# Optimization experiments

Hardware: AMD Instinct MI355X
Metric: run time of the kernel (lower is better)

## Reference

```python
import jax, jax.numpy as jnp
import numpy as np

N_NODES = 20000
EPS_BN = 1e-5
NEG_SLOPE = 0.2


def gat_conv(x, W, att_src, att_dst, bias, src, dst, heads, out_ch, concat):
    n = x.shape[0]
    h = (x @ W).reshape(n, heads, out_ch)                       # [N,H,C]
    a_src = jnp.sum(h * att_src, axis=-1)                       # [N,H]
    a_dst = jnp.sum(h * att_dst, axis=-1)                       # [N,H]
    e = jax.nn.leaky_relu(a_src[src] + a_dst[dst], NEG_SLOPE)   # [E,H]
    # segment softmax over incoming edges of each destination node
    m = jax.ops.segment_max(e, dst, num_segments=n)             # [N,H]
    e = jnp.exp(e - m[dst])
    denom = jax.ops.segment_sum(e, dst, num_segments=n)         # [N,H]
    alpha = e / (denom[dst] + 1e-16)                            # [E,H]
    msg = alpha[:, :, None] * h[src]                            # [E,H,C]
    out = jax.ops.segment_sum(msg, dst, num_segments=n)         # [N,H,C]
    if concat:
        out = out.reshape(n, heads * out_ch)
    else:
        out = out.mean(axis=1)
    return out + bias


def batch_norm(x, gamma, beta):
    mu = x.mean(axis=0)
    var = x.var(axis=0)  # biased, matches torch normalization
    return (x - mu) * jax.lax.rsqrt(var + EPS_BN) * gamma + beta


def setup_inputs() -> dict:
    key = jax.random.key(0)
    ks = jax.random.split(key, 16)
    n, d_in, hid, heads = N_NODES, 768, 128, 8
    n_edges = 160000
    x = jax.random.normal(ks[0], (n, d_in), dtype=jnp.float32)
    edge_index = jax.random.randint(ks[1], (2, n_edges), 0, n, dtype=jnp.int64)
    s = lambda fi, fo: (2.0 / (fi + fo)) ** 0.5
    return {
        "x": x,
        "edge_index": edge_index,
        "W1": jax.random.normal(ks[2], (d_in, heads * hid), jnp.float32) * s(d_in, heads * hid),
        "att_src1": jax.random.normal(ks[3], (heads, hid), jnp.float32) * 0.1,
        "att_dst1": jax.random.normal(ks[4], (heads, hid), jnp.float32) * 0.1,
        "bias1": jnp.zeros((heads * hid,), jnp.float32),
        "bn1_g": jnp.ones((heads * hid,), jnp.float32),
        "bn1_b": jnp.zeros((heads * hid,), jnp.float32),
        "W2": jax.random.normal(ks[5], (heads * hid, hid), jnp.float32) * s(heads * hid, hid),
        "att_src2": jax.random.normal(ks[6], (1, hid), jnp.float32) * 0.1,
        "att_dst2": jax.random.normal(ks[7], (1, hid), jnp.float32) * 0.1,
        "bias2": jnp.zeros((hid,), jnp.float32),
        "bn2_g": jnp.ones((hid,), jnp.float32),
        "bn2_b": jnp.zeros((hid,), jnp.float32),
        "Wc1": jax.random.normal(ks[8], (hid, 64), jnp.float32) * s(hid, 64),
        "bc1": jnp.zeros((64,), jnp.float32),
        "Wc2": jax.random.normal(ks[9], (64, 2), jnp.float32) * s(64, 2),
        "bc2": jnp.zeros((2,), jnp.float32),
    }


def reference(x, edge_index, W1, att_src1, att_dst1, bias1, bn1_g, bn1_b,
              W2, att_src2, att_dst2, bias2, bn2_g, bn2_b,
              Wc1, bc1, Wc2, bc2):
    n = x.shape[0]
    # PyG GATConv default: add self-loops
    loops = jnp.arange(n, dtype=edge_index.dtype)
    src = jnp.concatenate([edge_index[0], loops])
    dst = jnp.concatenate([edge_index[1], loops])

    h = gat_conv(x, W1, att_src1, att_dst1, bias1, src, dst, heads=8, out_ch=128, concat=True)
    h = jax.nn.elu(batch_norm(h, bn1_g, bn1_b))
    # dropout disabled (deterministic reference)
    h = gat_conv(h, W2, att_src2, att_dst2, bias2, src, dst, heads=1, out_ch=128, concat=False)
    h = jax.nn.elu(batch_norm(h, bn2_g, bn2_b))
    h = jax.nn.elu(h @ Wc1 + bc1)
    return h @ Wc2 + bc2  # [N, 2] logits
```

## Files before the change

### kernel.cpp

```cpp
#include <hip/hip_runtime.h>
#include <stdint.h>

typedef unsigned short u16;
typedef __bf16 bf16x8 __attribute__((ext_vector_type(8)));
typedef float f32x4 __attribute__((ext_vector_type(4)));

__device__ __forceinline__ float b2f(u16 u) {
    unsigned x = ((unsigned)u) << 16;
    return __builtin_bit_cast(float, x);
}
__device__ __forceinline__ u16 f2b(float f) {
    unsigned x = __builtin_bit_cast(unsigned, f);
    x = x + 0x7fffu + ((x >> 16) & 1u);
    return (u16)(x >> 16);
}
__device__ __forceinline__ float leaky(float v) { return v > 0.f ? v : 0.2f * v; }

__device__ __forceinline__ void gload16(const u16* g, u16* l) {
    __builtin_amdgcn_global_load_lds((const __attribute__((address_space(1))) void*)(const void*)g,
                                     (__attribute__((address_space(3))) void*)(void*)l, 16, 0, 0);
}

__global__ void k_cast4(const float* __restrict__ in, u16* __restrict__ out, size_t n4) {
    size_t i = blockIdx.x * (size_t)blockDim.x + threadIdx.x;
    size_t stride = (size_t)gridDim.x * blockDim.x;
    for (; i < n4; i += stride) {
        float4 v = ((const float4*)in)[i];
        ushort4 o;
        o.x = f2b(v.x); o.y = f2b(v.y); o.z = f2b(v.z); o.w = f2b(v.w);
        ((ushort4*)out)[i] = o;
    }
}

__global__ void k_tcast(const float* __restrict__ in, u16* __restrict__ out, int R, int C) {
    __shared__ float tile[32][33];
    int tx = threadIdx.x & 31, ty = threadIdx.x >> 5;
    int c0 = blockIdx.x * 32, r0 = blockIdx.y * 32;
    #pragma unroll
    for (int i = 0; i < 32; i += 8) {
        int r = r0 + ty + i, c = c0 + tx;
        tile[ty + i][tx] = (r < R && c < C) ? in[(size_t)r * C + c] : 0.f;
    }
    __syncthreads();
    #pragma unroll
    for (int i = 0; i < 32; i += 8) {
        int c = c0 + ty + i, r = r0 + tx;
        if (c < C && r < R) out[(size_t)c * R + r] = f2b(tile[tx][ty + i]);
    }
}

#define GBM 128
#define GBN 128
#define GBK 64

__global__ __launch_bounds__(256) void k_gemm(const u16* __restrict__ A, const u16* __restrict__ Bt,
                                              u16* __restrict__ C, int M, int NN, int K,
                                              const float* __restrict__ attS, const float* __restrict__ attD,
                                              float* __restrict__ asrc, float* __restrict__ adst, int HEADS) {
    __shared__ __align__(16) u16 As[GBM][GBK];
    __shared__ __align__(16) u16 Bs[GBN][GBK];
    __shared__ float redS[4][64];
    __shared__ float redD[4][64];
    int brow = blockIdx.x * GBM, bcol = blockIdx.y * GBN;
    int t = threadIdx.x, lane = t & 63, wid = t >> 6;
    int wm = (wid >> 1) * 64, wn = (wid & 1) * 64;
    int fr = lane & 15, fq = lane >> 4;
    f32x4 acc[4][4] = {};
    int srow = lane >> 3;
    int scol = (lane & 7) * 8;
    int nK = K / GBK;
    for (int kt = 0; kt < nK; ++kt) {
        int k0 = kt * GBK;
        #pragma unroll
        for (int cc = 0; cc < 8; ++cc) {
            int c = wid * 8 + cc;
            int r = (c & 15) * 8 + srow;
            if (c < 16) gload16(A + (size_t)(brow + r) * K + k0 + scol, &As[r][scol]);
            else        gload16(Bt + (size_t)(bcol + r) * K + k0 + scol, &Bs[r][scol]);
        }
        __syncthreads();
        #pragma unroll
        for (int kk = 0; kk < 2; ++kk) {
            int ko = kk * 32 + fq * 8;
            bf16x8 af[4], bg[4];
            #pragma unroll
            for (int i = 0; i < 4; ++i) {
                af[i] = *reinterpret_cast<const bf16x8*>(&As[wm + i * 16 + fr][ko]);
                bg[i] = *reinterpret_cast<const bf16x8*>(&Bs[wn + i * 16 + fr][ko]);
            }
            #pragma unroll
            for (int mi = 0; mi < 4; ++mi)
                #pragma unroll
                for (int ni = 0; ni < 4; ++ni)
                    acc[mi][ni] = __builtin_amdgcn_mfma_f32_16x16x32_bf16(af[mi], bg[ni], acc[mi][ni], 0, 0, 0);
        }
        __syncthreads();
    }
    #pragma unroll
    for (int mi = 0; mi < 4; ++mi) {
        #pragma unroll
        for (int j = 0; j < 4; ++j) {
            int row = brow + wm + mi * 16 + fq * 4 + j;
            if (row < M) {
                #pragma unroll
                for (int ni = 0; ni < 4; ++ni) {
                    int col = bcol + wn + ni * 16 + fr;
                    C[(size_t)row * NN + col] = f2b(acc[mi][ni][j]);
                }
            }
        }
    }
    if (attS != nullptr) {
        int head = blockIdx.y;
        const float* sv = attS + head * 128;
        const float* dv = attD + head * 128;
        float ps[4][4], pd[4][4];
        #pragma unroll
        for (int mi = 0; mi < 4; ++mi)
            #pragma unroll
            for (int j = 0; j < 4; ++j) {
                float s = 0.f, d = 0.f;
                #pragma unroll
                for (int ni = 0; ni < 4; ++ni) {
                    int lc = wn + ni * 16 + fr;
                    s += acc[mi][ni][j] * sv[lc];
                    d += acc[mi][ni][j] * dv[lc];
                }
                ps[mi][j] = s; pd[mi][j] = d;
            }
        #pragma unroll
        for (int mask = 1; mask < 16; mask <<= 1)
            #pragma unroll
            for (int mi = 0; mi < 4; ++mi)
                #pragma unroll
                for (int j = 0; j < 4; ++j) {
                    ps[mi][j] += __shfl_xor(ps[mi][j], mask);
                    pd[mi][j] += __shfl_xor(pd[mi][j], mask);
                }
        if (fr == 0) {
            #pragma unroll
            for (int mi = 0; mi < 4; ++mi)
                #pragma unroll
                for (int j = 0; j < 4; ++j) {
                    redS[wid][mi * 16 + fq * 4 + j] = ps[mi][j];
                    redD[wid][mi * 16 + fq * 4 + j] = pd[mi][j];
                }
        }
        __syncthreads();
        if ((wid & 1) == 0) {
            int row = brow + wm + lane;
            if (row < M) {
                asrc[(size_t)row * HEADS + head] = redS[wid][lane] + redS[wid | 1][lane];
                adst[(size_t)row * HEADS + head] = redD[wid][lane] + redD[wid | 1][lane];
            }
        }
    }
}

__global__ void k_detect(const int* __restrict__ ei, int* flag, int E0) {
    if (threadIdx.x == 0) *flag = 0;
    __syncthreads();
    int lim = E0 < 4096 ? E0 : 4096;
    int any = 0;
    for (int i = threadIdx.x; i < lim; i += 256) any |= (ei[2 * i + 1] != 0);
    if (any) atomicOr(flag, 1);
}

__global__ void k_deg(const int* __restrict__ ei, const int* __restrict__ flag,
                      int* __restrict__ deg, int E0, int E) {
    bool i64 = (*flag == 0);
    for (int e = blockIdx.x * blockDim.x + threadIdx.x; e < E; e += gridDim.x * blockDim.x) {
        int d;
        if (e < E0) d = i64 ? ei[2 * (E0 + e)] : ei[E0 + e];
        else d = e - E0;
        atomicAdd(&deg[d], 1);
    }
}

__global__ __launch_bounds__(1024) void k_scan(const int* __restrict__ deg, int* __restrict__ off,
                                               int* __restrict__ cursor, int n) {
    __shared__ int part[1024];
    int t = threadIdx.x;
    int chunk = (n + 1023) >> 10;
    int beg = t * chunk, end = beg + chunk;
    if (end > n) end = n;
    int s = 0;
    for (int i = beg; i < end; ++i) s += deg[i];
    part[t] = s;
    __syncthreads();
    for (int d = 1; d < 1024; d <<= 1) {
        int v = (t >= d) ? part[t - d] : 0;
        __syncthreads();
        part[t] += v;
        __syncthreads();
    }
    int run = (t == 0) ? 0 : part[t - 1];
    for (int i = beg; i < end; ++i) { off[i] = run; cursor[i] = run; run += deg[i]; }
    if (t == 1023) off[n] = part[1023];
}

__global__ void k_scatter(const int* __restrict__ ei, const int* __restrict__ flag,
                          int* __restrict__ cursor, int* __restrict__ csr, int E0, int E) {
    bool i64 = (*flag == 0);
    for (int e = blockIdx.x * blockDim.x + threadIdx.x; e < E; e += gridDim.x * blockDim.x) {
        int s, d;
        if (e < E0) {
            if (i64) { s = ei[2 * e]; d = ei[2 * (E0 + e)]; }
            else     { s = ei[e];     d = ei[E0 + e]; }
        } else { s = d = e - E0; }
        int pos = atomicAdd(&cursor[d], 1);
        csr[pos] = s;
    }
}

template <int HEADS>
__global__ __launch_bounds__(256) void k_alpha(const int* __restrict__ off, const int* __restrict__ csr,
                                               const float* __restrict__ asrc, const float* __restrict__ adst,
                                               float* __restrict__ pbuf, float* __restrict__ invb, int N) {
    const int EPC = 64 / HEADS;
    int t = threadIdx.x, lane = t & 63, wid = t >> 6;
    int node = blockIdx.x * 4 + wid;
    if (node >= N) return;
    int h = lane & (HEADS - 1);
    int e = lane / HEADS;
    float ad = adst[(size_t)node * HEADS + h];
    int lo = off[node], hi = off[node + 1];
    float m = -1e30f;
    for (int i = lo + e; i < hi; i += EPC) {
        int s = csr[i];
        float v = leaky(asrc[(size_t)s * HEADS + h] + ad);
        m = fmaxf(m, v);
    }
    #pragma unroll
    for (int mask = HEADS; mask < 64; mask <<= 1) m = fmaxf(m, __shfl_xor(m, mask));
    float ssum = 0.f;
    for (int i = lo + e; i < hi; i += EPC) {
        int s = csr[i];
        float v = leaky(asrc[(size_t)s * HEADS + h] + ad);
        float p = __expf(v - m);
        pbuf[(size_t)i * HEADS + h] = p;
        ssum += p;
    }
    #pragma unroll
    for (int mask = HEADS; mask < 64; mask <<= 1) ssum += __shfl_xor(ssum, mask);
    if (lane < HEADS) invb[(size_t)node * HEADS + h] = 1.f / (ssum + 1e-16f);
}

__global__ __launch_bounds__(256) void k_agg1(const int* __restrict__ off, const int* __restrict__ csr,
                                              const float* __restrict__ pbuf, const float* __restrict__ invb,
                                              const u16* __restrict__ h1, u16* __restrict__ outg, int N) {
    int node = blockIdx.x;
    if (node >= N) return;
    int t = threadIdx.x;
    int hh = t >> 5;
    int c0 = t * 4;
    int lo = off[node], hi = off[node + 1];
    float a0 = 0.f, a1 = 0.f, a2 = 0.f, a3 = 0.f;
    for (int i = lo; i < hi; ++i) {
        int s = csr[i];
        float p = pbuf[(size_t)i * 8 + hh];
        ushort4 u = *(const ushort4*)(h1 + (size_t)s * 1024 + c0);
        a0 += p * b2f(u.x); a1 += p * b2f(u.y);
        a2 += p * b2f(u.z); a3 += p * b2f(u.w);
    }
    float inv = invb[(size_t)node * 8 + hh];
    ushort4 o;
    o.x = f2b(a0 * inv); o.y = f2b(a1 * inv); o.z = f2b(a2 * inv); o.w = f2b(a3 * inv);
    *(ushort4*)(outg + (size_t)node * 1024 + c0) = o;
}

__global__ __launch_bounds__(256) void k_agg2(const int* __restrict__ off, const int* __restrict__ csr,
                                              const float* __restrict__ pbuf, const float* __restrict__ invb,
                                              const u16* __restrict__ h2, u16* __restrict__ outg, int N) {
    int t = threadIdx.x;
    int half = t >> 7, c = t & 127;
    int node = blockIdx.x * 2 + half;
    if (node >= N) return;
    int lo = off[node], hi = off[node + 1];
    float acc = 0.f;
    for (int i = lo; i < hi; ++i) {
        int s = csr[i];
        acc += pbuf[i] * b2f(h2[(size_t)s * 128 + c]);
    }
    outg[(size_t)node * 128 + c] = f2b(acc * invb[node]);
}

template <int CH>
__global__ __launch_bounds__(256) void k_bnpart(const u16* __restrict__ g, float* __restrict__ ps,
                                                float* __restrict__ ps2, int Nrows, int rowsPerChunk) {
    const int TPR = CH / 4;
    const int RPI = 256 / TPR;
    int t = threadIdx.x;
    int rl = t / TPR, c4 = (t % TPR) * 4;
    int chunk = blockIdx.x;
    int r0 = chunk * rowsPerChunk;
    int r1 = r0 + rowsPerChunk; if (r1 > Nrows) r1 = Nrows;
    float s[4] = {0.f, 0.f, 0.f, 0.f}, s2[4] = {0.f, 0.f, 0.f, 0.f};
    for (int r = r0 + rl; r < r1; r += RPI) {
        ushort4 u = *(const ushort4*)(g + (size_t)r * CH + c4);
        float v0 = b2f(u.x), v1 = b2f(u.y), v2 = b2f(u.z), v3 = b2f(u.w);
        s[0] += v0; s2[0] += v0 * v0;
        s[1] += v1; s2[1] += v1 * v1;
        s[2] += v2; s2[2] += v2 * v2;
        s[3] += v3; s2[3] += v3 * v3;
    }
    size_t prow = (size_t)(chunk * RPI + rl) * CH + c4;
    *(float4*)(ps + prow)  = make_float4(s[0], s[1], s[2], s[3]);
    *(float4*)(ps2 + prow) = make_float4(s2[0], s2[1], s2[2], s2[3]);
}

__global__ __launch_bounds__(256) void k_bnfinal(const float* __restrict__ ps, const float* __restrict__ ps2,
                                                 const float* __restrict__ gamma, const float* __restrict__ beta,
                                                 float* __restrict__ scale, float* __restrict__ shift,
                                                 int P, int CH, int Nrows) {
    int t = threadIdx.x, lane = t & 63, wid = t >> 6;
    int col = blockIdx.x * 4 + wid;
    if (col >= CH) return;
    float s = 0.f, s2 = 0.f;
    for (int p = lane; p < P; p += 64) {
        s += ps[(size_t)p * CH + col];
        s2 += ps2[(size_t)p * CH + col];
    }
    #pragma unroll
    for (int m = 1; m < 64; m <<= 1) { s += __shfl_xor(s, m); s2 += __shfl_xor(s2, m); }
    if (lane == 0) {
        double mu = (double)s / Nrows;
        double var = (double)s2 / Nrows - mu * mu;
        if (var < 0) var = 0;
        float sc = gamma[col] * rsqrtf((float)var + 1e-5f);
        scale[col] = sc;
        shift[col] = beta[col] - (float)mu * sc;
    }
}

__global__ void k_bn_elu(u16* __restrict__ g, const float* __restrict__ scale,
                         const float* __restrict__ shift, size_t total4, int CH) {
    size_t i = blockIdx.x * (size_t)blockDim.x + threadIdx.x;
    size_t stride = (size_t)gridDim.x * blockDim.x;
    for (; i < total4; i += stride) {
        size_t i4 = i * 4;
        int c0 = (int)(i4 % CH);
        ushort4 u = *(ushort4*)(g + i4);
        float v[4] = {b2f(u.x), b2f(u.y), b2f(u.z), b2f(u.w)};
        #pragma unroll
        for (int j = 0; j < 4; ++j) {
            float y = v[j] * scale[c0 + j] + shift[c0 + j];
            v[j] = y > 0.f ? y : expm1f(y);
        }
        ushort4 o;
        o.x = f2b(v[0]); o.y = f2b(v[1]); o.z = f2b(v[2]); o.w = f2b(v[3]);
        *(ushort4*)(g + i4) = o;
    }
}

__global__ __launch_bounds__(256) void k_cls(const u16* __restrict__ g2raw,
                                             const float* __restrict__ scale2, const float* __restrict__ shift2,
                                             const float* __restrict__ Wc1, const float* __restrict__ bc1,
                                             const float* __restrict__ Wc2, const float* __restrict__ bc2,
                                             float* __restrict__ out, int N) {
    __shared__ float wl[128 * 64];
    __shared__ float hs[4][128];
    int t = threadIdx.x, lane = t & 63, wid = t >> 6;
    for (int i = t; i < 128 * 64; i += 256) wl[i] = Wc1[i];
    float sc0 = scale2[2 * lane], sc1 = scale2[2 * lane + 1];
    float sh0 = shift2[2 * lane], sh1 = shift2[2 * lane + 1];
    float bb = bc1[lane];
    float c2a = Wc2[lane * 2], c2b = Wc2[lane * 2 + 1];
    float o2a = bc2[0], o2b = bc2[1];
    __syncthreads();
    int row0 = blockIdx.x * 64;
    for (int it = 0; it < 16; ++it) {
        int row = row0 + it * 4 + wid;
        if (row >= N) continue;
        const u16* hp = g2raw + (size_t)row * 128 + 2 * lane;
        float y0 = b2f(hp[0]) * sc0 + sh0; y0 = y0 > 0.f ? y0 : expm1f(y0);
        float y1 = b2f(hp[1]) * sc1 + sh1; y1 = y1 > 0.f ? y1 : expm1f(y1);
        hs[wid][2 * lane] = y0;
        hs[wid][2 * lane + 1] = y1;
        float tj = bb;
        #pragma unroll 8
        for (int c = 0; c < 128; ++c) tj += hs[wid][c] * wl[c * 64 + lane];
        tj = tj > 0.f ? tj : expm1f(tj);
        float v0 = tj * c2a, v1 = tj * c2b;
        #pragma unroll
        for (int m = 1; m < 64; m <<= 1) { v0 += __shfl_xor(v0, m); v1 += __shfl_xor(v1, m); }
        if (lane == 0) {
            out[(size_t)row * 2 + 0] = v0 + o2a;
            out[(size_t)row * 2 + 1] = v1 + o2b;
        }
    }
}

extern "C" void kernel_launch(void* const* d_in, const int* in_sizes, int n_in,
                              void* d_out, int out_size, void* d_ws, size_t ws_size,
                              hipStream_t stream) {
    const float* x     = (const float*)d_in[0];
    const int*   ei    = (const int*)d_in[1];
    const float* W1    = (const float*)d_in[2];
    const float* attS1 = (const float*)d_in[3];
    const float* attD1 = (const float*)d_in[4];
    const float* bn1g  = (const float*)d_in[6];
    const float* bn1b  = (const float*)d_in[7];
    const float* W2    = (const float*)d_in[8];
    const float* attS2 = (const float*)d_in[9];
    const float* attD2 = (const float*)d_in[10];
    const float* bn2g  = (const float*)d_in[12];
    const float* bn2b  = (const float*)d_in[13];
    const float* Wc1   = (const float*)d_in[14];
    const float* bc1   = (const float*)d_in[15];
    const float* Wc2   = (const float*)d_in[16];
    const float* bc2   = (const float*)d_in[17];
    float* out = (float*)d_out;

    const int DIN = 768, F1 = 1024, C2 = 128;
    const int N = in_sizes[0] / DIN;
    const int Mp = (N + GBM - 1) / GBM * GBM;
    const int E0 = in_sizes[1] / 2;
    const int E = E0 + N;

    char* w = (char*)d_ws;
    auto take = [&](size_t bytes) -> void* {
        void* p = (void*)w;
        w += (bytes + 255) & ~(size_t)255;
        return p;
    };
    u16* bufA   = (u16*)take((size_t)Mp * F1 * 2);
    u16* h1b    = (u16*)take((size_t)N * F1 * 2);
    u16* w1t    = (u16*)take((size_t)F1 * DIN * 2);
    u16* w2t    = (u16*)take((size_t)C2 * F1 * 2);
    float* asrc1 = (float*)take((size_t)N * 8 * 4);
    float* adst1 = (float*)take((size_t)N * 8 * 4);
    int* deg    = (int*)take((size_t)N * 4);
    int* off    = (int*)take((size_t)(N + 1) * 4);
    int* cursor = (int*)take((size_t)N * 4);
    int* csr    = (int*)take((size_t)E * 4);
    int* flag   = (int*)take(256);
    u16* h2b    = (u16*)take((size_t)N * C2 * 2);
    float* asrc2 = (float*)take((size_t)N * 4);
    float* adst2 = (float*)take((size_t)N * 4);
    u16* g2     = (u16*)take((size_t)N * C2 * 2);
    float* scale1 = (float*)take(F1 * 4);
    float* shift1 = (float*)take(F1 * 4);
    float* scale2 = (float*)take(C2 * 4);
    float* shift2 = (float*)take(C2 * 4);
    float* pbuf  = (float*)take((size_t)E * 8 * 4);
    float* invb1 = (float*)take((size_t)N * 8 * 4);
    float* invb2 = (float*)take((size_t)N * 4);
    float* psA   = (float*)take((size_t)1024 * 1024 * 4);
    float* psB   = (float*)take((size_t)1024 * 1024 * 4);

    hipMemsetAsync(deg, 0, (size_t)N * 4, stream);
    k_detect<<<1, 256, 0, stream>>>(ei, flag, E0);

    k_cast4<<<2048, 256, 0, stream>>>(x, bufA, (size_t)N * DIN / 4);
    k_tcast<<<dim3(F1 / 32, DIN / 32), 256, 0, stream>>>(W1, w1t, DIN, F1);
    k_tcast<<<dim3(C2 / 32, F1 / 32), 256, 0, stream>>>(W2, w2t, F1, C2);
    k_gemm<<<dim3(Mp / GBM, F1 / GBN), 256, 0, stream>>>(bufA, w1t, h1b, N, F1, DIN,
                                                         attS1, attD1, asrc1, adst1, 8);

    k_deg<<<512, 256, 0, stream>>>(ei, flag, deg, E0, E);
    k_scan<<<1, 1024, 0, stream>>>(deg, off, cursor, N);
    k_scatter<<<512, 256, 0, stream>>>(ei, flag, cursor, csr, E0, E);

    k_alpha<8><<<(N + 3) / 4, 256, 0, stream>>>(off, csr, asrc1, adst1, pbuf, invb1, N);
    k_agg1<<<N, 256, 0, stream>>>(off, csr, pbuf, invb1, h1b, bufA, N);
    {
        int nchunk = 256, rpc = (N + nchunk - 1) / nchunk;
        k_bnpart<1024><<<nchunk, 256, 0, stream>>>(bufA, psA, psB, N, rpc);
        k_bnfinal<<<F1 / 4, 256, 0, stream>>>(psA, psB, bn1g, bn1b, scale1, shift1, nchunk, F1, N);
    }
    k_bn_elu<<<4096, 256, 0, stream>>>(bufA, scale1, shift1, (size_t)N * F1 / 4, F1);

    k_gemm<<<dim3(Mp / GBM, C2 / GBN), 256, 0, stream>>>(bufA, w2t, h2b, N, C2, F1,
                                                         attS2, attD2, asrc2, adst2, 1);
    k_alpha<1><<<(N + 3) / 4, 256, 0, stream>>>(off, csr, asrc2, adst2, pbuf, invb2, N);
    k_agg2<<<(N + 1) / 2, 256, 0, stream>>>(off, csr, pbuf, invb2, h2b, g2, N);
    {
        int nchunk = 128, rpc = (N + nchunk - 1) / nchunk;
        k_bnpart<128><<<nchunk, 256, 0, stream>>>(g2, psA, psB, N, rpc);
        k_bnfinal<<<C2 / 4, 256, 0, stream>>>(psA, psB, bn2g, bn2b, scale2, shift2, nchunk * 8, C2, N);
    }

    k_cls<<<(N + 63) / 64, 256, 0, stream>>>(g2, scale2, shift2, Wc1, bc1, Wc2, bc2, out, N);
}
```

Before: 417.4 us.

## Fuse input cast and BN+ELU into GEMM A-loads; split attention dots out

The first GEMM now reads fp32 x directly and converts to bf16 while staging into LDS, which removes the separate cast kernel. The second GEMM applies the batch-norm scale/shift and ELU while loading A, which removes the standalone bn_elu pass over the 20000x1024 activation. Tile loads switch from async global_load_lds to register-staged loads into padded LDS rows, and the attention-score epilogue moves into separate small kernels that re-read h. The trade-offs are extra per-element ALU work in the GEMM load path, repeated transforms of A across column blocks, and the loss of direct-to-LDS loads.

```diff
diff --git a/kernel.cpp b/kernel.cpp
--- a/kernel.cpp
+++ b/kernel.cpp
@@ -15,22 +15,7 @@
     return (u16)(x >> 16);
 }
 __device__ __forceinline__ float leaky(float v) { return v > 0.f ? v : 0.2f * v; }
-
-__device__ __forceinline__ void gload16(const u16* g, u16* l) {
-    __builtin_amdgcn_global_load_lds((const __attribute__((address_space(1))) void*)(const void*)g,
-                                     (__attribute__((address_space(3))) void*)(void*)l, 16, 0, 0);
-}
-
-__global__ void k_cast4(const float* __restrict__ in, u16* __restrict__ out, size_t n4) {
-    size_t i = blockIdx.x * (size_t)blockDim.x + threadIdx.x;
-    size_t stride = (size_t)gridDim.x * blockDim.x;
-    for (; i < n4; i += stride) {
-        float4 v = ((const float4*)in)[i];
-        ushort4 o;
-        o.x = f2b(v.x); o.y = f2b(v.y); o.z = f2b(v.z); o.w = f2b(v.w);
-        ((ushort4*)out)[i] = o;
-    }
-}
+__device__ __forceinline__ float elu(float v) { return v > 0.f ? v : expm1f(v); }
 
 __global__ void k_tcast(const float* __restrict__ in, u16* __restrict__ out, int R, int C) {
     __shared__ float tile[32][33];
@@ -52,31 +37,68 @@
 #define GBM 128
 #define GBN 128
 #define GBK 64
-
-__global__ __launch_bounds__(256) void k_gemm(const u16* __restrict__ A, const u16* __restrict__ Bt,
+#define LDT 72
+
+template <int AMODE>
+__global__ __launch_bounds__(256) void k_gemm(const void* __restrict__ Araw, const u16* __restrict__ Bt,
                                               u16* __restrict__ C, int M, int NN, int K,
-                                              const float* __restrict__ attS, const float* __restrict__ attD,
-                                              float* __restrict__ asrc, float* __restrict__ adst, int HEADS) {
-    __shared__ __align__(16) u16 As[GBM][GBK];
-    __shared__ __align__(16) u16 Bs[GBN][GBK];
-    __shared__ float redS[4][64];
-    __shared__ float redD[4][64];
+                                              const float* __restrict__ scA, const float* __restrict__ shA) {
+    __shared__ __align__(16) u16 As[GBM][LDT];
+    __shared__ __align__(16) u16 Bs[GBN][LDT];
     int brow = blockIdx.x * GBM, bcol = blockIdx.y * GBN;
-    int t = threadIdx.x, lane = t & 63, wid = t >> 6;
+    int t = threadIdx.x;
+    int lane = t & 63, wid = t >> 6;
     int wm = (wid >> 1) * 64, wn = (wid & 1) * 64;
     int fr = lane & 15, fq = lane >> 4;
     f32x4 acc[4][4] = {};
-    int srow = lane >> 3;
-    int scol = (lane & 7) * 8;
+    int tr = t >> 3, tc = (t & 7) * 8;
     int nK = K / GBK;
     for (int kt = 0; kt < nK; ++kt) {
         int k0 = kt * GBK;
         #pragma unroll
-        for (int cc = 0; cc < 8; ++cc) {
-            int c = wid * 8 + cc;
-            int r = (c & 15) * 8 + srow;
-            if (c < 16) gload16(A + (size_t)(brow + r) * K + k0 + scol, &As[r][scol]);
-            else        gload16(Bt + (size_t)(bcol + r) * K + k0 + scol, &Bs[r][scol]);
+        for (int rr = 0; rr < 4; ++rr) {
+            int r = tr + rr * 32;
+            int grow = brow + r;
+            uint4 bv = *reinterpret_cast<const uint4*>(Bt + (size_t)(bcol + r) * K + k0 + tc);
+            *reinterpret_cast<uint4*>(&Bs[r][tc]) = bv;
+            uint4 av = make_uint4(0, 0, 0, 0);
+            if (AMODE == 0) {
+                if (grow < M) av = *reinterpret_cast<const uint4*>((const u16*)Araw + (size_t)grow * K + k0 + tc);
+            } else if (AMODE == 1) {
+                if (grow < M) {
+                    const float* ap = (const float*)Araw + (size_t)grow * K + k0 + tc;
+                    float4 a0 = *(const float4*)ap;
+                    float4 a1 = *(const float4*)(ap + 4);
+                    ushort4 lo, hi;
+                    lo.x = f2b(a0.x); lo.y = f2b(a0.y); lo.z = f2b(a0.z); lo.w = f2b(a0.w);
+                    hi.x = f2b(a1.x); hi.y = f2b(a1.y); hi.z = f2b(a1.z); hi.w = f2b(a1.w);
+                    av.x = (unsigned)lo.x | ((unsigned)lo.y << 16);
+                    av.y = (unsigned)lo.z | ((unsigned)lo.w << 16);
+                    av.z = (unsigned)hi.x | ((unsigned)hi.y << 16);
+                    av.w = (unsigned)hi.z | ((unsigned)hi.w << 16);
+                }
+            } else {
+                if (grow < M) {
+                    uint4 u = *reinterpret_cast<const uint4*>((const u16*)Araw + (size_t)grow * K + k0 + tc);
+                    float4 s0 = *(const float4*)(scA + k0 + tc);
+                    float4 s1 = *(const float4*)(scA + k0 + tc + 4);
+                    float4 h0 = *(const float4*)(shA + k0 + tc);
+                    float4 h1 = *(const float4*)(shA + k0 + tc + 4);
+                    u16 w0 = f2b(elu(b2f((u16)(u.x & 0xffff)) * s0.x + h0.x));
+                    u16 w1 = f2b(elu(b2f((u16)(u.x >> 16))    * s0.y + h0.y));
+                    u16 w2 = f2b(elu(b2f((u16)(u.y & 0xffff)) * s0.z + h0.z));
+                    u16 w3 = f2b(elu(b2f((u16)(u.y >> 16))    * s0.w + h0.w));
+                    u16 w4 = f2b(elu(b2f((u16)(u.z & 0xffff)) * s1.x + h1.x));
+                    u16 w5 = f2b(elu(b2f((u16)(u.z >> 16))    * s1.y + h1.y));
+                    u16 w6 = f2b(elu(b2f((u16)(u.w & 0xffff)) * s1.z + h1.z));
+                    u16 w7 = f2b(elu(b2f((u16)(u.w >> 16))    * s1.w + h1.w));
+                    av.x = (unsigned)w0 | ((unsigned)w1 << 16);
+                    av.y = (unsigned)w2 | ((unsigned)w3 << 16);
+                    av.z = (unsigned)w4 | ((unsigned)w5 << 16);
+                    av.w = (unsigned)w6 | ((unsigned)w7 << 16);
+                }
+            }
+            *reinterpret_cast<uint4*>(&As[r][tc]) = av;
         }
         __syncthreads();
         #pragma unroll
@@ -110,51 +132,45 @@
             }
         }
     }
-    if (attS != nullptr) {
-        int head = blockIdx.y;
-        const float* sv = attS + head * 128;
-        const float* dv = attD + head * 128;
-        float ps[4][4], pd[4][4];
-        #pragma unroll
-        for (int mi = 0; mi < 4; ++mi)
-            #pragma unroll
-            for (int j = 0; j < 4; ++j) {
-                float s = 0.f, d = 0.f;
-                #pragma unroll
-                for (int ni = 0; ni < 4; ++ni) {
-                    int lc = wn + ni * 16 + fr;
-                    s += acc[mi][ni][j] * sv[lc];
-                    d += acc[mi][ni][j] * dv[lc];
-                }
-                ps[mi][j] = s; pd[mi][j] = d;
-            }
-        #pragma unroll
-        for (int mask = 1; mask < 16; mask <<= 1)
-            #pragma unroll
-            for (int mi = 0; mi < 4; ++mi)
-                #pragma unroll
-                for (int j = 0; j < 4; ++j) {
-                    ps[mi][j] += __shfl_xor(ps[mi][j], mask);
-                    pd[mi][j] += __shfl_xor(pd[mi][j], mask);
-                }
-        if (fr == 0) {
-            #pragma unroll
-            for (int mi = 0; mi < 4; ++mi)
-                #pragma unroll
-                for (int j = 0; j < 4; ++j) {
-                    redS[wid][mi * 16 + fq * 4 + j] = ps[mi][j];
-                    redD[wid][mi * 16 + fq * 4 + j] = pd[mi][j];
-                }
-        }
-        __syncthreads();
-        if ((wid & 1) == 0) {
-            int row = brow + wm + lane;
-            if (row < M) {
-                asrc[(size_t)row * HEADS + head] = redS[wid][lane] + redS[wid | 1][lane];
-                adst[(size_t)row * HEADS + head] = redD[wid][lane] + redD[wid | 1][lane];
-            }
-        }
-    }
+}
+
+__global__ void k_att8(const u16* __restrict__ h, const float* __restrict__ attS,
+                       const float* __restrict__ attD, float* __restrict__ asrc,
+                       float* __restrict__ adst, int N) {
+    int t = threadIdx.x;
+    int half = t >> 7, i = t & 127;
+    int row = blockIdx.x * 2 + half;
+    if (row >= N) return;
+    int head = i >> 4, g = i & 15;
+    const u16* hp = h + (size_t)row * 1024 + head * 128 + g * 8;
+    const float* sp = attS + head * 128 + g * 8;
+    const float* dp = attD + head * 128 + g * 8;
+    ushort4 u0 = *(const ushort4*)hp;
+    ushort4 u1 = *(const ushort4*)(hp + 4);
+    float hv[8] = {b2f(u0.x), b2f(u0.y), b2f(u0.z), b2f(u0.w),
+                   b2f(u1.x), b2f(u1.y), b2f(u1.z), b2f(u1.w)};
+    float ps = 0.f, pd = 0.f;
+    #pragma unroll
+    for (int j = 0; j < 8; ++j) { ps += hv[j] * sp[j]; pd += hv[j] * dp[j]; }
+    #pragma unroll
+    for (int m = 1; m < 16; m <<= 1) { ps += __shfl_xor(ps, m); pd += __shfl_xor(pd, m); }
+    if (g == 0) { asrc[row * 8 + head] = ps; adst[row * 8 + head] = pd; }
+}
+
+__global__ void k_att1(const u16* __restrict__ h, const float* __restrict__ attS,
+                       const float* __restrict__ attD, float* __restrict__ asrc,
+                       float* __restrict__ adst, int N) {
+    int t = threadIdx.x;
+    int wid = t >> 6, lane = t & 63;
+    int row = blockIdx.x * 4 + wid;
+    if (row >= N) return;
+    const u16* hp = h + (size_t)row * 128 + lane * 2;
+    float h0 = b2f(hp[0]), h1 = b2f(hp[1]);
+    float ps = h0 * attS[lane * 2] + h1 * attS[lane * 2 + 1];
+    float pd = h0 * attD[lane * 2] + h1 * attD[lane * 2 + 1];
+    #pragma unroll
+    for (int m = 1; m < 64; m <<= 1) { ps += __shfl_xor(ps, m); pd += __shfl_xor(pd, m); }
+    if (lane == 0) { asrc[row] = ps; adst[row] = pd; }
 }
 
 __global__ void k_detect(const int* __restrict__ ei, int* flag, int E0) {
@@ -330,26 +346,6 @@
         float sc = gamma[col] * rsqrtf((float)var + 1e-5f);
         scale[col] = sc;
         shift[col] = beta[col] - (float)mu * sc;
-    }
-}
-
-__global__ void k_bn_elu(u16* __restrict__ g, const float* __restrict__ scale,
-                         const float* __restrict__ shift, size_t total4, int CH) {
-    size_t i = blockIdx.x * (size_t)blockDim.x + threadIdx.x;
-    size_t stride = (size_t)gridDim.x * blockDim.x;
-    for (; i < total4; i += stride) {
-        size_t i4 = i * 4;
-        int c0 = (int)(i4 % CH);
-        ushort4 u = *(ushort4*)(g + i4);
-        float v[4] = {b2f(u.x), b2f(u.y), b2f(u.z), b2f(u.w)};
-        #pragma unroll
-        for (int j = 0; j < 4; ++j) {
-            float y = v[j] * scale[c0 + j] + shift[c0 + j];
-            v[j] = y > 0.f ? y : expm1f(y);
-        }
-        ushort4 o;
-        o.x = f2b(v[0]); o.y = f2b(v[1]); o.z = f2b(v[2]); o.w = f2b(v[3]);
-        *(ushort4*)(g + i4) = o;
     }
 }
 
@@ -414,9 +410,9 @@
 
     const int DIN = 768, F1 = 1024, C2 = 128;
     const int N = in_sizes[0] / DIN;
-    const int Mp = (N + GBM - 1) / GBM * GBM;
     const int E0 = in_sizes[1] / 2;
     const int E = E0 + N;
+    const int nMB = (N + GBM - 1) / GBM;
 
     char* w = (char*)d_ws;
     auto take = [&](size_t bytes) -> void* {
@@ -424,7 +420,7 @@
         w += (bytes + 255) & ~(size_t)255;
         return p;
     };
-    u16* bufA   = (u16*)take((size_t)Mp * F1 * 2);
+    u16* bufA   = (u16*)take((size_t)N * F1 * 2);
     u16* h1b    = (u16*)take((size_t)N * F1 * 2);
     u16* w1t    = (u16*)take((size_t)F1 * DIN * 2);
     u16* w2t    = (u16*)take((size_t)C2 * F1 * 2);
@@ -452,11 +448,11 @@
     hipMemsetAsync(deg, 0, (size_t)N * 4, stream);
     k_detect<<<1, 256, 0, stream>>>(ei, flag, E0);
 
-    k_cast4<<<2048, 256, 0, stream>>>(x, bufA, (size_t)N * DIN / 4);
     k_tcast<<<dim3(F1 / 32, DIN / 32), 256, 0, stream>>>(W1, w1t, DIN, F1);
     k_tcast<<<dim3(C2 / 32, F1 / 32), 256, 0, stream>>>(W2, w2t, F1, C2);
-    k_gemm<<<dim3(Mp / GBM, F1 / GBN), 256, 0, stream>>>(bufA, w1t, h1b, N, F1, DIN,
-                                                         attS1, attD1, asrc1, adst1, 8);
+
+    k_gemm<1><<<dim3(nMB, F1 / GBN), 256, 0, stream>>>(x, w1t, h1b, N, F1, DIN, nullptr, nullptr);
+    k_att8<<<(N + 1) / 2, 256, 0, stream>>>(h1b, attS1, attD1, asrc1, adst1, N);
 
     k_deg<<<512, 256, 0, stream>>>(ei, flag, deg, E0, E);
     k_scan<<<1, 1024, 0, stream>>>(deg, off, cursor, N);
@@ -469,10 +465,10 @@
         k_bnpart<1024><<<nchunk, 256, 0, stream>>>(bufA, psA, psB, N, rpc);
         k_bnfinal<<<F1 / 4, 256, 0, stream>>>(psA, psB, bn1g, bn1b, scale1, shift1, nchunk, F1, N);
     }
-    k_bn_elu<<<4096, 256, 0, stream>>>(bufA, scale1, shift1, (size_t)N * F1 / 4, F1);
-
-    k_gemm<<<dim3(Mp / GBM, C2 / GBN), 256, 0, stream>>>(bufA, w2t, h2b, N, C2, F1,
-                                                         attS2, attD2, asrc2, adst2, 1);
+
+    k_gemm<2><<<dim3(nMB, C2 / GBN), 256, 0, stream>>>(bufA, w2t, h2b, N, C2, F1, scale1, shift1);
+    k_att1<<<(N + 3) / 4, 256, 0, stream>>>(h2b, attS2, attD2, asrc2, adst2, N);
+
     k_alpha<1><<<(N + 3) / 4, 256, 0, stream>>>(off, csr, asrc2, adst2, pbuf, invb2, N);
     k_agg2<<<(N + 1) / 2, 256, 0, stream>>>(off, csr, pbuf, invb2, h2b, g2, N);
     {
```

New measurement: 462.3 us. +10.8%, slower.
